# Kernel tuning notes

Hardware: AMD Instinct MI355X
Metric: run time of the kernel (lower is better)

## Reference

```python
import jax, jax.numpy as jnp
import numpy as np
import math

B, N, H, QLEN, VLEN = 4, 2048, 16, 64, 64


def setup_inputs() -> dict:
    key = jax.random.key(0)
    k1, k2, k3, k4 = jax.random.split(key, 4)
    return {
        "queries": jax.random.normal(k1, (B, N, QLEN * H), dtype=jnp.float32),
        "keys": jax.random.normal(k2, (B, N, QLEN * H), dtype=jnp.float32),
        "values": jax.random.normal(k3, (B, N, VLEN * H), dtype=jnp.float32),
        "neuron_bank_connectivity_sub": jax.random.uniform(k4, (1, 1, N, N), dtype=jnp.float32),
    }


def reference(queries, keys, values, neuron_bank_connectivity_sub):
    b, n, _ = queries.shape
    # separate_attention_heads: view(B, N, vec_len, H) then permute to [B, H, N, vec_len]
    q = queries.reshape(b, n, QLEN, H).transpose(0, 3, 1, 2)   # bhnq
    k = keys.reshape(b, n, QLEN, H).transpose(0, 3, 1, 2)      # bhmq
    scores = jnp.einsum("bhnq,bhmq->bhnm", q, k) / math.sqrt(QLEN)
    probs = jax.nn.softmax(scores - neuron_bank_connectivity_sub, axis=-1)
    v = values.reshape(b, n, VLEN, H).transpose(0, 3, 1, 2)    # bhmv
    attn_out = jnp.einsum("bhnm,bhmv->bhnv", probs, v)          # [B, H, N, VLEN]
    # Faithful to original: .view on the [B,H,N,V]-contiguous tensor (flat reinterpret),
    # NOT the permuted copy.
    return attn_out.reshape(b, n, H * VLEN)
```

## Files before the change

### kernel.cpp

```cpp
#include <hip/hip_runtime.h>
#include <stdint.h>

#define B_ 4
#define N_ 2048
#define H_ 16
#define D_ 64
#define LOG2E 1.44269504088896f

typedef unsigned short u16;
typedef __attribute__((ext_vector_type(8))) short short8;
typedef __attribute__((ext_vector_type(16))) float f32x16;

#if __has_builtin(__builtin_amdgcn_exp2f)
#define EXP2(x) __builtin_amdgcn_exp2f(x)
#else
#define EXP2(x) exp2f(x)
#endif

__device__ __forceinline__ u16 f2bf(float f){
  union { float f; uint32_t u; } c; c.f = f;
  return (u16)((c.u + 0x7FFFu + ((c.u >> 16) & 1u)) >> 16);
}
__device__ __forceinline__ uint32_t cvtpk(float lo, float hi){
  uint32_t r; asm("v_cvt_pk_bf16_f32 %0, %1, %2" : "=v"(r) : "v"(lo), "v"(hi)); return r;
}
__device__ __forceinline__ void pl32swap(uint32_t &a, uint32_t &b){
  asm("v_permlane32_swap_b32 %0, %1" : "+v"(a), "+v"(b));
}
__device__ __forceinline__ void llds16(const void* g, void* l){
  __builtin_amdgcn_global_load_lds((const __attribute__((address_space(1))) void*)g,
                                   (__attribute__((address_space(3))) void*)l, 16, 0, 0);
}
__device__ __forceinline__ int csw(int c){ return c ^ ((c >> 6) << 1); }

__global__ __launch_bounds__(256) void repack_qkv(const float* __restrict__ q,
    const float* __restrict__ k, const float* __restrict__ v,
    u16* __restrict__ Qb, u16* __restrict__ Kb, u16* __restrict__ VTb){
  __shared__ u16 tile[16][1026];
  const int blk = blockIdx.x;
  const int b = blk >> 7, nt = blk & 127;
  const int n0 = nt * 16;
  const int t = threadIdx.x;

  for (int pass = 0; pass < 3; ++pass){
    const float* src = pass==0 ? q : (pass==1 ? k : v);
    const float scale = (pass==0) ? 0.125f*LOG2E : 1.0f;
    if (pass) __syncthreads();
#pragma unroll
    for (int j = 0; j < 16; ++j){
      const float4 f = ((const float4*)(src + ((size_t)(b*N_ + n0 + j))*1024))[t];
      const int c = csw(4*t);
      tile[j][c^0] = f2bf(f.x*scale); tile[j][c^1] = f2bf(f.y*scale);
      tile[j][c^2] = f2bf(f.z*scale); tile[j][c^3] = f2bf(f.w*scale);
    }
    __syncthreads();
    if (pass < 2){
      u16* dstT = (pass==0) ? Qb : Kb;
#pragma unroll
      for (int i2 = 0; i2 < 8; ++i2){
        const int id = t + i2*256;
        const int g = id & 7, nn = (id>>3) & 15, h = id >> 7;
        union { u16 b[8]; short8 s; } r8;
#pragma unroll
        for (int jj = 0; jj < 8; ++jj) r8.b[jj] = tile[nn][csw((g*8+jj)*16 + h)];
        *(short8*)(dstT + ((size_t)(b*H_+h)*N_ + n0+nn)*D_ + g*8) = r8.s;
      }
    } else {
#pragma unroll
      for (int i2 = 0; i2 < 8; ++i2){
        const int id = t + i2*256;
        const int gn = id & 1, d = (id>>1) & 63, h = id >> 7;
        union { u16 b[8]; short8 s; } r8;
#pragma unroll
        for (int jj = 0; jj < 8; ++jj) r8.b[jj] = tile[gn*8+jj][csw(d*16+h)];
        *(short8*)(VTb + ((size_t)(b*H_+h)*D_ + d)*N_ + n0 + gn*8) = r8.s;
      }
    }
  }
}

__global__ __launch_bounds__(256) void repack_biasb(const float* __restrict__ bias,
                                                    u16* __restrict__ bB){
  const int id = blockIdx.x*256 + threadIdx.x;
  const int hi = id & 1, n = (id>>1) & (N_-1), mb = id >> 12;
  const float* src = bias + (size_t)n*N_ + mb*64 + 4*hi;
  uint32_t w[16];
#pragma unroll
  for (int g2 = 0; g2 < 8; ++g2){
    float4 f = *(const float4*)(src + g2*8);
    w[2*g2+0] = cvtpk(-LOG2E*f.x, -LOG2E*f.y);
    w[2*g2+1] = cvtpk(-LOG2E*f.z, -LOG2E*f.w);
  }
  uint4* dst = (uint4*)(bB + (size_t)id*32);
#pragma unroll
  for (int g4 = 0; g4 < 4; ++g4)
    dst[g4] = make_uint4(w[4*g4], w[4*g4+1], w[4*g4+2], w[4*g4+3]);
}

__global__ __launch_bounds__(256, 2) void attn_kernel(
    const u16* __restrict__ Qb, const u16* __restrict__ Kb,
    const u16* __restrict__ VTb, const u16* __restrict__ bB,
    float* __restrict__ out){
  __shared__ u16 K_sh[2*64*64];
  __shared__ u16 V_sh[2*64*64];

  const int tid = threadIdx.x;
  const int strip = tid >> 6, lane = tid & 63;
  const int ln = lane & 31, hi = lane >> 5;
  const int bx = blockIdx.x;
  const int qt = bx & 7, ch = bx >> 3;
  const int h  = ch & 15;
  const int b  = ch >> 4;
  const int bh = b*H_ + h;
  const int nq0 = qt*256 + strip*64 + ln;

  short8 qf0[4], qf1[4];
  {
    const u16* qb0 = Qb + ((size_t)bh*N_ + nq0)*D_;
#pragma unroll
    for (int kc = 0; kc < 4; ++kc){
      qf0[kc] = *(const short8*)(qb0 + kc*16 + hi*8);
      qf1[kc] = *(const short8*)(qb0 + 32*D_ + kc*16 + hi*8);
    }
  }

  f32x16 O00, O01, O10, O11;
#pragma unroll
  for (int i = 0; i < 16; ++i){ O00[i]=0.f; O01[i]=0.f; O10[i]=0.f; O11[i]=0.f; }
  float lrun0 = 0.f, lrun1 = 0.f;

  const size_t Kg = (size_t)bh*N_*D_;
  const size_t Vg = (size_t)bh*D_*N_;
  const int r0b = strip*16;
  const int srow = lane >> 3, sb = lane & 7;
  const size_t bB0 = ((size_t)nq0*2 + hi)*32;

  uint32_t bn0[16], bn1[16];
#pragma unroll
  for (int cc = 0; cc < 2; ++cc){
    const int r0 = r0b + cc*8;
    const int rowk = r0 + srow;
    llds16(Kb + Kg + (size_t)rowk*D_ + ((sb ^ (rowk&7))<<3), (void*)(K_sh + r0*64));
    llds16(VTb + Vg + (size_t)rowk*N_ + ((sb ^ (rowk&7))<<3), (void*)(V_sh + r0*64));
  }
  {
    const uint4* bp = (const uint4*)(bB + bB0);
#pragma unroll
    for (int g4 = 0; g4 < 4; ++g4){
      uint4 a = bp[g4], c = bp[g4 + 256];
      bn0[4*g4]=a.x; bn0[4*g4+1]=a.y; bn0[4*g4+2]=a.z; bn0[4*g4+3]=a.w;
      bn1[4*g4]=c.x; bn1[4*g4+1]=c.y; bn1[4*g4+2]=c.z; bn1[4*g4+3]=c.w;
    }
  }
  __syncthreads();

  for (int it = 0; it < 32; ++it){
    const int cur = it & 1;
    const u16* Kslab = K_sh + cur*4096;
    const u16* Vslab = V_sh + cur*4096;

    if (it < 31){
      const int m1 = (it+1)*64;
      u16* Kd = K_sh + (cur^1)*4096;
      u16* Vd = V_sh + (cur^1)*4096;
#pragma unroll
      for (int cc = 0; cc < 2; ++cc){
        const int r0 = r0b + cc*8;
        const int rowk = r0 + srow;
        llds16(Kb + Kg + (size_t)(m1+rowk)*D_ + ((sb ^ (rowk&7))<<3), (void*)(Kd + r0*64));
        llds16(VTb + Vg + (size_t)rowk*N_ + m1 + ((sb ^ (rowk&7))<<3), (void*)(Vd + r0*64));
      }
    }

    f32x16 st00, st01, st10, st11;
#pragma unroll
    for (int k2 = 0; k2 < 8; ++k2){
      st00[2*k2]   = __uint_as_float(bn0[k2]   << 16);
      st00[2*k2+1] = __uint_as_float(bn0[k2]   & 0xffff0000u);
      st01[2*k2]   = __uint_as_float(bn0[k2+8] << 16);
      st01[2*k2+1] = __uint_as_float(bn0[k2+8] & 0xffff0000u);
      st10[2*k2]   = __uint_as_float(bn1[k2]   << 16);
      st10[2*k2+1] = __uint_as_float(bn1[k2]   & 0xffff0000u);
      st11[2*k2]   = __uint_as_float(bn1[k2+8] << 16);
      st11[2*k2+1] = __uint_as_float(bn1[k2+8] & 0xffff0000u);
    }
    if (it < 31){
      const uint4* bp = (const uint4*)(bB + (size_t)(it+1)*N_*64 + bB0);
#pragma unroll
      for (int g4 = 0; g4 < 4; ++g4){
        uint4 a = bp[g4], c = bp[g4 + 256];
        bn0[4*g4]=a.x; bn0[4*g4+1]=a.y; bn0[4*g4+2]=a.z; bn0[4*g4+3]=a.w;
        bn1[4*g4]=c.x; bn1[4*g4+1]=c.y; bn1[4*g4+2]=c.z; bn1[4*g4+3]=c.w;
      }
    }

#pragma unroll
    for (int kc = 0; kc < 4; ++kc){
      const short8 k0 = *(const short8*)(Kslab + ln*64      + (((kc*2+hi) ^ (ln&7))<<3));
      const short8 k1 = *(const short8*)(Kslab + (32+ln)*64 + (((kc*2+hi) ^ ((32+ln)&7))<<3));
      st00 = __builtin_amdgcn_mfma_f32_32x32x16_bf16(k0, qf0[kc], st00, 0,0,0);
      st01 = __builtin_amdgcn_mfma_f32_32x32x16_bf16(k1, qf0[kc], st01, 0,0,0);
      st10 = __builtin_amdgcn_mfma_f32_32x32x16_bf16(k0, qf1[kc], st10, 0,0,0);
      st11 = __builtin_amdgcn_mfma_f32_32x32x16_bf16(k1, qf1[kc], st11, 0,0,0);
    }

    {
      float ps0=0.f, ps1=0.f, ps2=0.f, ps3=0.f;
#pragma unroll
      for (int r = 0; r < 16; ++r){
        const float p0 = EXP2(st00[r]); st00[r] = p0;
        const float p1 = EXP2(st01[r]); st01[r] = p1;
        if (r & 1){ ps1 += p0; ps3 += p1; } else { ps0 += p0; ps2 += p1; }
      }
      float psum = (ps0 + ps1) + (ps2 + ps3);
      psum += __shfl_xor(psum, 32);
      lrun0 += psum;
    }

#pragma unroll
    for (int mc = 0; mc < 4; ++mc){
      const int c8 = (mc & 1)*8;
      uint32_t a0,a1,a2,a3;
      if (mc < 2){
        a0 = cvtpk(st00[c8+0], st00[c8+1]); a1 = cvtpk(st00[c8+2], st00[c8+3]);
        a2 = cvtpk(st00[c8+4], st00[c8+5]); a3 = cvtpk(st00[c8+6], st00[c8+7]);
      } else {
        a0 = cvtpk(st01[c8+0], st01[c8+1]); a1 = cvtpk(st01[c8+2], st01[c8+3]);
        a2 = cvtpk(st01[c8+4], st01[c8+5]); a3 = cvtpk(st01[c8+6], st01[c8+7]);
      }
      pl32swap(a0, a2); pl32swap(a1, a3);
      union { uint32_t u[4]; short8 s; } pf;
      pf.u[0]=a0; pf.u[1]=a1; pf.u[2]=a2; pf.u[3]=a3;
      const short8 v0 = *(const short8*)(Vslab + ln*64      + (((mc*2+hi) ^ (ln&7))<<3));
      const short8 v1 = *(const short8*)(Vslab + (32+ln)*64 + (((mc*2+hi) ^ ((32+ln)&7))<<3));
      O00 = __builtin_amdgcn_mfma_f32_32x32x16_bf16(v0, pf.s, O00, 0,0,0);
      O01 = __builtin_amdgcn_mfma_f32_32x32x16_bf16(v1, pf.s, O01, 0,0,0);
    }

    {
      float ps0=0.f, ps1=0.f, ps2=0.f, ps3=0.f;
#pragma unroll
      for (int r = 0; r < 16; ++r){
        const float p0 = EXP2(st10[r]); st10[r] = p0;
        const float p1 = EXP2(st11[r]); st11[r] = p1;
        if (r & 1){ ps1 += p0; ps3 += p1; } else { ps0 += p0; ps2 += p1; }
      }
      float psum = (ps0 + ps1) + (ps2 + ps3);
      psum += __shfl_xor(psum, 32);
      lrun1 += psum;
    }

#pragma unroll
    for (int mc = 0; mc < 4; ++mc){
      const int c8 = (mc & 1)*8;
      uint32_t b0,b1,b2,b3;
      if (mc < 2){
        b0 = cvtpk(st10[c8+0], st10[c8+1]); b1 = cvtpk(st10[c8+2], st10[c8+3]);
        b2 = cvtpk(st10[c8+4], st10[c8+5]); b3 = cvtpk(st10[c8+6], st10[c8+7]);
      } else {
        b0 = cvtpk(st11[c8+0], st11[c8+1]); b1 = cvtpk(st11[c8+2], st11[c8+3]);
        b2 = cvtpk(st11[c8+4], st11[c8+5]); b3 = cvtpk(st11[c8+6], st11[c8+7]);
      }
      pl32swap(b0, b2); pl32swap(b1, b3);
      union { uint32_t u[4]; short8 s; } pf;
      pf.u[0]=b0; pf.u[1]=b1; pf.u[2]=b2; pf.u[3]=b3;
      const short8 v0 = *(const short8*)(Vslab + ln*64      + (((mc*2+hi) ^ (ln&7))<<3));
      const short8 v1 = *(const short8*)(Vslab + (32+ln)*64 + (((mc*2+hi) ^ ((32+ln)&7))<<3));
      O10 = __builtin_amdgcn_mfma_f32_32x32x16_bf16(v0, pf.s, O10, 0,0,0);
      O11 = __builtin_amdgcn_mfma_f32_32x32x16_bf16(v1, pf.s, O11, 0,0,0);
    }
    __syncthreads();
  }

  const float inv0 = 1.0f / lrun0;
  const float inv1 = 1.0f / lrun1;
  float* ob0 = out + ((size_t)bh*N_ + nq0)*D_;
  float* ob1 = ob0 + 32*D_;
#pragma unroll
  for (int g2 = 0; g2 < 4; ++g2){
    float4 a = make_float4(O00[4*g2]*inv0, O00[4*g2+1]*inv0, O00[4*g2+2]*inv0, O00[4*g2+3]*inv0);
    float4 c = make_float4(O01[4*g2]*inv0, O01[4*g2+1]*inv0, O01[4*g2+2]*inv0, O01[4*g2+3]*inv0);
    *(float4*)(ob0 + 8*g2 + 4*hi)      = a;
    *(float4*)(ob0 + 8*g2 + 4*hi + 32) = c;
    float4 d = make_float4(O10[4*g2]*inv1, O10[4*g2+1]*inv1, O10[4*g2+2]*inv1, O10[4*g2+3]*inv1);
    float4 e = make_float4(O11[4*g2]*inv1, O11[4*g2+1]*inv1, O11[4*g2+2]*inv1, O11[4*g2+3]*inv1);
    *(float4*)(ob1 + 8*g2 + 4*hi)      = d;
    *(float4*)(ob1 + 8*g2 + 4*hi + 32) = e;
  }
}

extern "C" void kernel_launch(void* const* d_in, const int* in_sizes, int n_in,
                              void* d_out, int out_size, void* d_ws, size_t ws_size,
                              hipStream_t stream) {
  const float* q    = (const float*)d_in[0];
  const float* k    = (const float*)d_in[1];
  const float* v    = (const float*)d_in[2];
  const float* bias = (const float*)d_in[3];

  const size_t TEN = (size_t)B_*H_*N_*D_;
  u16* Qb  = (u16*)d_ws;
  u16* Kb  = Qb + TEN;
  u16* VTb = Kb + TEN;
  u16* bB  = VTb + TEN;

  repack_qkv<<<B_*128, 256, 0, stream>>>(q, k, v, Qb, Kb, VTb);
  repack_biasb<<<512, 256, 0, stream>>>(bias, bB);
  attn_kernel<<<512, 256, 0, stream>>>(Qb, Kb, VTb, bB, (float*)d_out);
}
```

Measured before the change: 134.8 us.

## Split key range across two blocks and combine partial attention outputs

Templates the attention kernel so each query tile can process only half of the key sequence. This doubles the grid to 1024 blocks, and each block writes unnormalized partial outputs and row sums to workspace. A new combine kernel adds the two partials and normalizes them. The aim is more parallelism and better load balance, at the cost of extra global traffic for the partial buffers and one more launch. The old single-pass path is kept as a fallback when the workspace is too small.

After: 199.9 us. 48.3% more time.

```diff
diff --git a/kernel.cpp b/kernel.cpp
--- a/kernel.cpp
+++ b/kernel.cpp
@@ -6,6 +6,8 @@
 #define H_ 16
 #define D_ 64
 #define LOG2E 1.44269504088896f
+#define ROWS_ (B_*H_*N_)
+#define OUTELEMS_ ((size_t)ROWS_*D_)
 
 typedef unsigned short u16;
 typedef __attribute__((ext_vector_type(8))) short short8;
@@ -97,10 +99,11 @@
     dst[g4] = make_uint4(w[4*g4], w[4*g4+1], w[4*g4+2], w[4*g4+3]);
 }
 
+template<int SPLIT>
 __global__ __launch_bounds__(256, 2) void attn_kernel(
     const u16* __restrict__ Qb, const u16* __restrict__ Kb,
     const u16* __restrict__ VTb, const u16* __restrict__ bB,
-    float* __restrict__ out){
+    float* __restrict__ outp, float* __restrict__ pL){
   __shared__ u16 K_sh[2*64*64];
   __shared__ u16 V_sh[2*64*64];
 
@@ -108,11 +111,15 @@
   const int strip = tid >> 6, lane = tid & 63;
   const int ln = lane & 31, hi = lane >> 5;
   const int bx = blockIdx.x;
-  const int qt = bx & 7, ch = bx >> 3;
+  const int sx  = SPLIT ? (bx >> 9) : 0;
+  const int rem = SPLIT ? (bx & 511) : bx;
+  const int qt = rem & 7, ch = rem >> 3;
   const int h  = ch & 15;
   const int b  = ch >> 4;
   const int bh = b*H_ + h;
   const int nq0 = qt*256 + strip*64 + ln;
+  const int it0 = sx * (SPLIT ? 16 : 0);
+  const int itN = SPLIT ? 16 : 32;
 
   short8 qf0[4], qf1[4];
   {
@@ -136,15 +143,18 @@
   const size_t bB0 = ((size_t)nq0*2 + hi)*32;
 
   uint32_t bn0[16], bn1[16];
-#pragma unroll
-  for (int cc = 0; cc < 2; ++cc){
-    const int r0 = r0b + cc*8;
-    const int rowk = r0 + srow;
-    llds16(Kb + Kg + (size_t)rowk*D_ + ((sb ^ (rowk&7))<<3), (void*)(K_sh + r0*64));
-    llds16(VTb + Vg + (size_t)rowk*N_ + ((sb ^ (rowk&7))<<3), (void*)(V_sh + r0*64));
-  }
   {
-    const uint4* bp = (const uint4*)(bB + bB0);
+    const int mb0 = it0*64;
+#pragma unroll
+    for (int cc = 0; cc < 2; ++cc){
+      const int r0 = r0b + cc*8;
+      const int rowk = r0 + srow;
+      llds16(Kb + Kg + (size_t)(mb0+rowk)*D_ + ((sb ^ (rowk&7))<<3), (void*)(K_sh + r0*64));
+      llds16(VTb + Vg + (size_t)rowk*N_ + mb0 + ((sb ^ (rowk&7))<<3), (void*)(V_sh + r0*64));
+    }
+  }
+  {
+    const uint4* bp = (const uint4*)(bB + (size_t)it0*N_*64 + bB0);
 #pragma unroll
     for (int g4 = 0; g4 < 4; ++g4){
       uint4 a = bp[g4], c = bp[g4 + 256];
@@ -154,12 +164,14 @@
   }
   __syncthreads();
 
-  for (int it = 0; it < 32; ++it){
-    const int cur = it & 1;
+#pragma unroll 1
+  for (int ii = 0; ii < itN; ++ii){
+    const int it = it0 + ii;
+    const int cur = ii & 1;
     const u16* Kslab = K_sh + cur*4096;
     const u16* Vslab = V_sh + cur*4096;
 
-    if (it < 31){
+    if (ii < itN-1){
       const int m1 = (it+1)*64;
       u16* Kd = K_sh + (cur^1)*4096;
       u16* Vd = V_sh + (cur^1)*4096;
@@ -184,7 +196,7 @@
       st11[2*k2]   = __uint_as_float(bn1[k2+8] << 16);
       st11[2*k2+1] = __uint_as_float(bn1[k2+8] & 0xffff0000u);
     }
-    if (it < 31){
+    if (ii < itN-1){
       const uint4* bp = (const uint4*)(bB + (size_t)(it+1)*N_*64 + bB0);
 #pragma unroll
       for (int g4 = 0; g4 < 4; ++g4){
@@ -272,21 +284,45 @@
     __syncthreads();
   }
 
-  const float inv0 = 1.0f / lrun0;
-  const float inv1 = 1.0f / lrun1;
-  float* ob0 = out + ((size_t)bh*N_ + nq0)*D_;
-  float* ob1 = ob0 + 32*D_;
-#pragma unroll
-  for (int g2 = 0; g2 < 4; ++g2){
-    float4 a = make_float4(O00[4*g2]*inv0, O00[4*g2+1]*inv0, O00[4*g2+2]*inv0, O00[4*g2+3]*inv0);
-    float4 c = make_float4(O01[4*g2]*inv0, O01[4*g2+1]*inv0, O01[4*g2+2]*inv0, O01[4*g2+3]*inv0);
-    *(float4*)(ob0 + 8*g2 + 4*hi)      = a;
-    *(float4*)(ob0 + 8*g2 + 4*hi + 32) = c;
-    float4 d = make_float4(O10[4*g2]*inv1, O10[4*g2+1]*inv1, O10[4*g2+2]*inv1, O10[4*g2+3]*inv1);
-    float4 e = make_float4(O11[4*g2]*inv1, O11[4*g2+1]*inv1, O11[4*g2+2]*inv1, O11[4*g2+3]*inv1);
-    *(float4*)(ob1 + 8*g2 + 4*hi)      = d;
-    *(float4*)(ob1 + 8*g2 + 4*hi + 32) = e;
-  }
+  if (SPLIT){
+    float* ob0 = outp + (size_t)sx*OUTELEMS_ + ((size_t)bh*N_ + nq0)*D_;
+    float* ob1 = ob0 + 32*D_;
+#pragma unroll
+    for (int g2 = 0; g2 < 4; ++g2){
+      *(float4*)(ob0 + 8*g2 + 4*hi)      = make_float4(O00[4*g2],O00[4*g2+1],O00[4*g2+2],O00[4*g2+3]);
+      *(float4*)(ob0 + 8*g2 + 4*hi + 32) = make_float4(O01[4*g2],O01[4*g2+1],O01[4*g2+2],O01[4*g2+3]);
+      *(float4*)(ob1 + 8*g2 + 4*hi)      = make_float4(O10[4*g2],O10[4*g2+1],O10[4*g2+2],O10[4*g2+3]);
+      *(float4*)(ob1 + 8*g2 + 4*hi + 32) = make_float4(O11[4*g2],O11[4*g2+1],O11[4*g2+2],O11[4*g2+3]);
+    }
+    if (hi == 0){
+      pL[(size_t)sx*ROWS_ + bh*N_ + nq0]      = lrun0;
+      pL[(size_t)sx*ROWS_ + bh*N_ + nq0 + 32] = lrun1;
+    }
+  } else {
+    const float inv0 = 1.0f / lrun0;
+    const float inv1 = 1.0f / lrun1;
+    float* ob0 = outp + ((size_t)bh*N_ + nq0)*D_;
+    float* ob1 = ob0 + 32*D_;
+#pragma unroll
+    for (int g2 = 0; g2 < 4; ++g2){
+      *(float4*)(ob0 + 8*g2 + 4*hi)      = make_float4(O00[4*g2]*inv0,O00[4*g2+1]*inv0,O00[4*g2+2]*inv0,O00[4*g2+3]*inv0);
+      *(float4*)(ob0 + 8*g2 + 4*hi + 32) = make_float4(O01[4*g2]*inv0,O01[4*g2+1]*inv0,O01[4*g2+2]*inv0,O01[4*g2+3]*inv0);
+      *(float4*)(ob1 + 8*g2 + 4*hi)      = make_float4(O10[4*g2]*inv1,O10[4*g2+1]*inv1,O10[4*g2+2]*inv1,O10[4*g2+3]*inv1);
+      *(float4*)(ob1 + 8*g2 + 4*hi + 32) = make_float4(O11[4*g2]*inv1,O11[4*g2+1]*inv1,O11[4*g2+2]*inv1,O11[4*g2+3]*inv1);
+    }
+  }
+}
+
+__global__ __launch_bounds__(256) void combine_k(const float* __restrict__ pO,
+    const float* __restrict__ pL, float* __restrict__ out){
+  const size_t gid = (size_t)blockIdx.x*256 + threadIdx.x;
+  const size_t e4 = gid*4;
+  const size_t row = e4 >> 6;
+  const float inv = 1.0f / (pL[row] + pL[ROWS_ + row]);
+  const float4 a = *(const float4*)(pO + e4);
+  const float4 b = *(const float4*)(pO + OUTELEMS_ + e4);
+  *(float4*)(out + e4) = make_float4((a.x+b.x)*inv, (a.y+b.y)*inv,
+                                     (a.z+b.z)*inv, (a.w+b.w)*inv);
 }
 
 extern "C" void kernel_launch(void* const* d_in, const int* in_sizes, int n_in,
@@ -302,8 +338,16 @@
   u16* Kb  = Qb + TEN;
   u16* VTb = Kb + TEN;
   u16* bB  = VTb + TEN;
+  float* pO = (float*)(bB + (size_t)N_*N_);
+  float* pL = pO + 2*OUTELEMS_;
+  const size_t need = (3*TEN + (size_t)N_*N_)*2 + (2*OUTELEMS_ + 2*ROWS_)*4;
 
   repack_qkv<<<B_*128, 256, 0, stream>>>(q, k, v, Qb, Kb, VTb);
   repack_biasb<<<512, 256, 0, stream>>>(bias, bB);
-  attn_kernel<<<512, 256, 0, stream>>>(Qb, Kb, VTb, bB, (float*)d_out);
-}
+  if (ws_size >= need){
+    attn_kernel<1><<<1024, 256, 0, stream>>>(Qb, Kb, VTb, bB, pO, pL);
+    combine_k<<<8192, 256, 0, stream>>>(pO, pL, (float*)d_out);
+  } else {
+    attn_kernel<0><<<512, 256, 0, stream>>>(Qb, Kb, VTb, bB, (float*)d_out, nullptr);
+  }
+}
```
